# Kernel optimization log

Measured on AMD Instinct MI355X. Metric: run time of the kernel, lower is better.

Reference implementation:

```python
import jax, jax.numpy as jnp
import numpy as np
import math

B, N, DS, DP, DH, H, PQK, PV = 1, 384, 384, 128, 16, 12, 4, 8
PKV = PQK + PV
EPS = 1e-8
SOFTPLUS_INV_1 = 0.541324854612918


def setup_inputs() -> dict:
    key = jax.random.key(0)
    ks = jax.random.split(key, 20)
    W = lambda k, shp: (jax.random.normal(k, shp, dtype=jnp.float32) * 0.02)
    s = jax.random.normal(ks[0], (B, N, DS), dtype=jnp.float32)
    z = jax.random.normal(ks[1], (B, N, N, DP), dtype=jnp.float32)
    # random rigid frames: orthonormal rotations via QR + translations
    rot = jnp.linalg.qr(jax.random.normal(ks[2], (B, N, 3, 3), dtype=jnp.float32))[0]
    trans = jax.random.normal(ks[3], (B, N, 3), dtype=jnp.float32)
    square_mask = jnp.zeros((B, 1, N, N), dtype=jnp.float32)
    HC = H * DH
    COUT = H * (DP + DH + PV * 4)  # 2112
    return {
        "s": s, "z": z, "rot": rot, "trans": trans, "square_mask": square_mask,
        "Wq": W(ks[4], (DS, HC)), "bq": jnp.zeros((HC,), jnp.float32),
        "Wkv": W(ks[5], (DS, 2 * HC)), "bkv": jnp.zeros((2 * HC,), jnp.float32),
        "Wq_pts": W(ks[6], (DS, H * PQK * 3)), "bq_pts": jnp.zeros((H * PQK * 3,), jnp.float32),
        "Wkv_pts": W(ks[7], (DS, H * PKV * 3)), "bkv_pts": jnp.zeros((H * PKV * 3,), jnp.float32),
        "Wb": W(ks[8], (DP, H)), "bb": jnp.zeros((H,), jnp.float32),
        "head_weights": jnp.full((H,), SOFTPLUS_INV_1, dtype=jnp.float32),
        "Wout": W(ks[9], (COUT, DS)), "bout": jnp.zeros((DS,), jnp.float32),
    }


def _points(lin, rot, trans, npts):
    # lin: [B,N,3*H*npts] laid out as 3 coord-chunks of H*npts each (torch split+stack)
    pts = jnp.swapaxes(lin.reshape(B, N, 3, H * npts), -1, -2)  # [B,N,H*npts,3]
    pts = jnp.einsum('bnij,bnpj->bnpi', rot, pts) + trans[:, :, None, :]  # frame apply
    return pts.reshape(B, N, H, npts, 3)


def reference(s, z, rot, trans, square_mask, Wq, bq, Wkv, bkv, Wq_pts, bq_pts,
              Wkv_pts, bkv_pts, Wb, bb, head_weights, Wout, bout):
    q = (s @ Wq + bq).reshape(B, N, H, DH)
    kv = (s @ Wkv + bkv).reshape(B, N, H, 2 * DH)
    k, v = kv[..., :DH], kv[..., DH:]

    q_pts = _points(s @ Wq_pts + bq_pts, rot, trans, PQK)          # [B,N,H,PQK,3]
    kv_pts = _points(s @ Wkv_pts + bkv_pts, rot, trans, PKV)       # [B,N,H,PKV,3]
    k_pts, v_pts = kv_pts[..., :PQK, :], kv_pts[..., PQK:, :]

    bias = z @ Wb + bb                                             # [B,Nq,Nk,H]
    attn = jnp.einsum('bqhd,bkhd->bhqk', q, k) * math.sqrt(1.0 / (3 * DH))
    attn = attn + math.sqrt(1.0 / 3) * jnp.transpose(bias, (0, 3, 1, 2))

    diff = q_pts[:, :, None] - k_pts[:, None]                      # [B,Nq,Nk,H,PQK,3]
    dist2 = jnp.sum(diff * diff, axis=-1)                          # [B,Nq,Nk,H,PQK]
    hw = jax.nn.softplus(head_weights) * math.sqrt(1.0 / (3 * (PQK * 9.0 / 2)))
    pt_att = -0.5 * jnp.sum(dist2 * hw[None, None, None, :, None], axis=-1)  # [B,Nq,Nk,H]

    attn = attn + square_mask + jnp.transpose(pt_att, (0, 3, 1, 2))
    attn = jax.nn.softmax(attn, axis=-1)                           # [B,H,Nq,Nk]

    o = jnp.einsum('bhqk,bkhd->bqhd', attn, v).reshape(B, N, H * DH)
    o_pts = jnp.einsum('bhqk,bkhpc->bqhpc', attn, v_pts)           # [B,N,H,PV,3]
    # frame invert_apply: R^T (p - t)
    o_pts = jnp.einsum('bnji,bnhpj->bnhpi', rot, o_pts - trans[:, :, None, None, :])
    o_pts_norm = jnp.sqrt(jnp.sum(o_pts ** 2, axis=-1) + EPS).reshape(B, N, H * PV)
    o_pts_flat = o_pts.reshape(B, N, H * PV, 3)
    o_pair = jnp.einsum('bhqk,bqkc->bqhc', attn, z).reshape(B, N, H * DP)

    cat = jnp.concatenate(
        [o, o_pts_flat[..., 0], o_pts_flat[..., 1], o_pts_flat[..., 2], o_pts_norm, o_pair],
        axis=-1)
    return cat @ Wout + bout
```

## Files before the change

kernel.cpp:

```cpp
#include <hip/hip_runtime.h>
#include <math.h>

#define N     384
#define DSd   384
#define DP    128
#define DH    16
#define H     12
#define PQK   4
#define PV    8
#define HC    (H*DH)
#define PROJW 1152
#define NN    (N*N)
#define COUTD 2112
#define KSPL  4
#define KCH   96

__global__ __launch_bounds__(256) void pack_w(
    const float* __restrict__ Wq, const float* __restrict__ Wkv,
    const float* __restrict__ Wqp, const float* __restrict__ Wkvp,
    const float* __restrict__ bq, const float* __restrict__ bkv,
    const float* __restrict__ bqp, const float* __restrict__ bkvp,
    float* __restrict__ Wcat, float* __restrict__ bcat)
{
    const int i = blockIdx.x * 256 + threadIdx.x;
    if (i < DSd * PROJW) {
        const int r = i / PROJW, c = i % PROJW;
        float v;
        if (c < 192)      v = Wq[r*192 + c];
        else if (c < 576) v = Wkv[r*384 + (c-192)];
        else if (c < 720) v = Wqp[r*144 + (c-576)];
        else              v = Wkvp[r*432 + (c-720)];
        Wcat[i] = v;
    }
    if (i < PROJW) {
        float v;
        if (i < 192)      v = bq[i];
        else if (i < 576) v = bkv[i-192];
        else if (i < 720) v = bqp[i-576];
        else              v = bkvp[i-720];
        bcat[i] = v;
    }
}

__global__ __launch_bounds__(256) void gemm32x64(
    const float* __restrict__ A, const float* __restrict__ B,
    float* __restrict__ partial, int M, int Nc, int K, int kchunk)
{
    __shared__ float Ast[32][34];
    __shared__ float Bs[32][68];
    const int tid = threadIdx.x;
    const int tc = tid & 15, tr = tid >> 4;
    const int row0 = blockIdx.x * 32, col0 = blockIdx.y * 64;
    const int kbeg = blockIdx.z * kchunk;
    const int kend = kbeg + kchunk;
    float acc[2][4] = {};

    for (int kk = kbeg; kk < kend; kk += 32) {
        #pragma unroll
        for (int i = tid; i < 32*32; i += 256) {
            int r = i >> 5, c = i & 31;
            Ast[c][r] = A[(row0 + r) * K + kk + c];
        }
        #pragma unroll
        for (int i = tid; i < 32*64; i += 256) {
            int r = i >> 6, c = i & 63;
            Bs[r][c] = B[(kk + r) * Nc + col0 + c];
        }
        __syncthreads();
        #pragma unroll
        for (int p = 0; p < 32; ++p) {
            const float2 av = *(const float2*)&Ast[p][tr*2];
            const float4 bv = *(const float4*)&Bs[p][tc*4];
            acc[0][0] = fmaf(av.x, bv.x, acc[0][0]);
            acc[0][1] = fmaf(av.x, bv.y, acc[0][1]);
            acc[0][2] = fmaf(av.x, bv.z, acc[0][2]);
            acc[0][3] = fmaf(av.x, bv.w, acc[0][3]);
            acc[1][0] = fmaf(av.y, bv.x, acc[1][0]);
            acc[1][1] = fmaf(av.y, bv.y, acc[1][1]);
            acc[1][2] = fmaf(av.y, bv.z, acc[1][2]);
            acc[1][3] = fmaf(av.y, bv.w, acc[1][3]);
        }
        __syncthreads();
    }
    float* p0 = partial + ((size_t)blockIdx.z * M + row0 + tr*2) * Nc + col0 + tc*4;
    *(float4*)p0        = make_float4(acc[0][0], acc[0][1], acc[0][2], acc[0][3]);
    *(float4*)(p0 + Nc) = make_float4(acc[1][0], acc[1][1], acc[1][2], acc[1][3]);
}

__global__ __launch_bounds__(256) void reduce_kernel(
    const float* __restrict__ partial, const float* __restrict__ bias,
    float* __restrict__ out, int nc, int parts, int stride)
{
    const int i = blockIdx.x * 256 + threadIdx.x;
    float a = bias[i % nc];
    for (int t = 0; t < parts; ++t) a += partial[(size_t)t * stride + i];
    out[i] = a;
}

__global__ __launch_bounds__(192) void repack_kernel(
    const float* __restrict__ proj, const float* __restrict__ rot,
    const float* __restrict__ trans,
    float* __restrict__ q_t, float* __restrict__ k_t, float* __restrict__ vcat,
    float* __restrict__ qpts_t, float* __restrict__ kpts_t)
{
    const int n = blockIdx.x;
    const int tid = threadIdx.x;
    const float* pr = proj + n * PROJW;

    {
        int h = tid >> 4, d = tid & 15;
        q_t[(h*N + n)*DH + d]   = pr[h*DH + d];
        k_t[(h*N + n)*DH + d]   = pr[HC + h*2*DH + d];
        vcat[(h*N + n)*40 + d]  = pr[HC + h*2*DH + DH + d];
    }
    const float r00 = rot[n*9+0], r01 = rot[n*9+1], r02 = rot[n*9+2];
    const float r10 = rot[n*9+3], r11 = rot[n*9+4], r12 = rot[n*9+5];
    const float r20 = rot[n*9+6], r21 = rot[n*9+7], r22 = rot[n*9+8];
    const float t0 = trans[n*3+0], t1 = trans[n*3+1], t2 = trans[n*3+2];

    if (tid < H*PQK) {
        int p = tid;
        float l0 = pr[576 + 0*48 + p];
        float l1 = pr[576 + 1*48 + p];
        float l2 = pr[576 + 2*48 + p];
        int h = p / PQK, pt = p % PQK;
        float* dst = qpts_t + (h*N + n)*12 + pt*3;
        dst[0] = r00*l0 + r01*l1 + r02*l2 + t0;
        dst[1] = r10*l0 + r11*l1 + r12*l2 + t1;
        dst[2] = r20*l0 + r21*l1 + r22*l2 + t2;
    }
    if (tid < H*(PQK+PV)) {
        int p = tid;
        float l0 = pr[720 + 0*144 + p];
        float l1 = pr[720 + 1*144 + p];
        float l2 = pr[720 + 2*144 + p];
        int h = p / 12, pt = p % 12;
        float x0 = r00*l0 + r01*l1 + r02*l2 + t0;
        float x1 = r10*l0 + r11*l1 + r12*l2 + t1;
        float x2 = r20*l0 + r21*l1 + r22*l2 + t2;
        if (pt < PQK) {
            float* dst = kpts_t + (h*N + n)*12 + pt*3;
            dst[0] = x0; dst[1] = x1; dst[2] = x2;
        } else {
            float* dst = vcat + (h*N + n)*40 + 16 + (pt - PQK)*3;
            dst[0] = x0; dst[1] = x1; dst[2] = x2;
        }
    }
}

__global__ __launch_bounds__(256) void bias_kernel(
    const float* __restrict__ z, const float* __restrict__ Wb,
    const float* __restrict__ bb, float* __restrict__ biasattn)
{
    __shared__ float zt[64][DP+1];
    const int tid = threadIdx.x;
    const int base = blockIdx.x * 64;
    for (int i = tid; i < 64*DP; i += 256)
        zt[i >> 7][i & 127] = z[(size_t)base*DP + i];
    __syncthreads();

    const int p = tid & 63;
    const int g3 = __builtin_amdgcn_readfirstlane((tid >> 6) * 3);
    float a0 = 0.f, a1 = 0.f, a2 = 0.f;
    #pragma unroll 4
    for (int c = 0; c < DP; ++c) {
        float zv = zt[p][c];
        a0 = fmaf(zv, Wb[c*H + g3 + 0], a0);
        a1 = fmaf(zv, Wb[c*H + g3 + 1], a1);
        a2 = fmaf(zv, Wb[c*H + g3 + 2], a2);
    }
    const float sc = 0.5773502691896258f;
    const int pair = base + p;
    biasattn[(g3+0)*NN + pair] = (a0 + bb[g3+0]) * sc;
    biasattn[(g3+1)*NN + pair] = (a1 + bb[g3+1]) * sc;
    biasattn[(g3+2)*NN + pair] = (a2 + bb[g3+2]) * sc;
}

__global__ __launch_bounds__(128) void attn_kernel(
    const float* __restrict__ q_t, const float* __restrict__ k_t,
    const float* __restrict__ qpts_t, const float* __restrict__ kpts_t,
    const float* __restrict__ mask, const float* __restrict__ head_weights,
    float* __restrict__ biasattn)
{
    const int h  = blockIdx.x % H;
    const int qi = blockIdx.x / H;
    const int tid = threadIdx.x;
    __shared__ float logits[N];
    __shared__ float red[4];

    const float4* qv = (const float4*)(q_t + (h*N + qi)*DH);
    const float4 q0 = qv[0], q1 = qv[1], q2 = qv[2], q3 = qv[3];
    const float4* qpv = (const float4*)(qpts_t + (h*N + qi)*12);
    const float4 p0 = qpv[0], p1 = qpv[1], p2 = qpv[2];
    const float hw = log1pf(expf(head_weights[h])) * 0.13608276348795434f;

    float lmax = -1e30f;
    for (int k = tid; k < N; k += 128) {
        const float4* kr = (const float4*)(k_t + (h*N + k)*DH);
        const float4 a0 = kr[0], a1 = kr[1], a2 = kr[2], a3 = kr[3];
        float dot = q0.x*a0.x;
        dot = fmaf(q0.y, a0.y, dot); dot = fmaf(q0.z, a0.z, dot); dot = fmaf(q0.w, a0.w, dot);
        dot = fmaf(q1.x, a1.x, dot); dot = fmaf(q1.y, a1.y, dot); dot = fmaf(q1.z, a1.z, dot); dot = fmaf(q1.w, a1.w, dot);
        dot = fmaf(q2.x, a2.x, dot); dot = fmaf(q2.y, a2.y, dot); dot = fmaf(q2.z, a2.z, dot); dot = fmaf(q2.w, a2.w, dot);
        dot = fmaf(q3.x, a3.x, dot); dot = fmaf(q3.y, a3.y, dot); dot = fmaf(q3.z, a3.z, dot); dot = fmaf(q3.w, a3.w, dot);
        const float4* kp = (const float4*)(kpts_t + (h*N + k)*12);
        const float4 b0 = kp[0], b1 = kp[1], b2 = kp[2];
        float df, d2;
        df = p0.x-b0.x; d2 = df*df;
        df = p0.y-b0.y; d2 = fmaf(df, df, d2);
        df = p0.z-b0.z; d2 = fmaf(df, df, d2);
        df = p0.w-b0.w; d2 = fmaf(df, df, d2);
        df = p1.x-b1.x; d2 = fmaf(df, df, d2);
        df = p1.y-b1.y; d2 = fmaf(df, df, d2);
        df = p1.z-b1.z; d2 = fmaf(df, df, d2);
        df = p1.w-b1.w; d2 = fmaf(df, df, d2);
        df = p2.x-b2.x; d2 = fmaf(df, df, d2);
        df = p2.y-b2.y; d2 = fmaf(df, df, d2);
        df = p2.z-b2.z; d2 = fmaf(df, df, d2);
        df = p2.w-b2.w; d2 = fmaf(df, df, d2);
        float l = fmaf(dot, 0.14433756729740643f,
                       biasattn[h*NN + qi*N + k] + mask[qi*N + k])
                - 0.5f * hw * d2;
        logits[k] = l;
        lmax = fmaxf(lmax, l);
    }
    #pragma unroll
    for (int o = 32; o > 0; o >>= 1) lmax = fmaxf(lmax, __shfl_xor(lmax, o));
    if ((tid & 63) == 0) red[tid >> 6] = lmax;
    __syncthreads();
    const float m = fmaxf(red[0], red[1]);
    float lsum = 0.f;
    for (int k = tid; k < N; k += 128) {
        float e = __expf(logits[k] - m);
        logits[k] = e;
        lsum += e;
    }
    #pragma unroll
    for (int o = 32; o > 0; o >>= 1) lsum += __shfl_xor(lsum, o);
    if ((tid & 63) == 0) red[2 + (tid >> 6)] = lsum;
    __syncthreads();
    const float inv = 1.f / (red[2] + red[3]);
    for (int k = tid; k < N; k += 128)
        biasattn[h*NN + qi*N + k] = logits[k] * inv;
}

__global__ __launch_bounds__(256) void opair_partial(
    const float* __restrict__ attn, const float* __restrict__ vcat,
    const float* __restrict__ z, float* __restrict__ P1, float* __restrict__ P2)
{
    const int qi = blockIdx.x, kq = blockIdx.y;
    const int k0 = kq * KCH;
    const int tid = threadIdx.x;
    __shared__ float pzs[2][H][DP];

    {
        const int c = tid & 127;
        const int halfu = __builtin_amdgcn_readfirstlane(tid >> 7);
        const float* zp = z + ((size_t)qi*N + k0 + halfu*48)*DP + c;
        float zreg[48];
        #pragma unroll
        for (int k = 0; k < 48; ++k) zreg[k] = zp[(size_t)k*DP];
        const float* arow = attn + qi*N + k0 + halfu*48;
        #pragma unroll
        for (int h = 0; h < H; ++h) {
            float a = 0.f;
            #pragma unroll
            for (int k = 0; k < 48; ++k)
                a = fmaf(arow[h*NN + k], zreg[k], a);
            pzs[halfu][h][c] = a;
        }
    }
    {
        const int wv = tid >> 6, lane = tid & 63;
        if (lane < 40) {
            #pragma unroll
            for (int ih = 0; ih < 3; ++ih) {
                const int h = wv*3 + ih;
                const float* arow2 = attn + h*NN + qi*N + k0;
                const float* vp = vcat + ((size_t)h*N + k0)*40 + lane;
                float a = 0.f;
                #pragma unroll 4
                for (int k = 0; k < KCH; ++k)
                    a = fmaf(arow2[k], vp[k*40], a);
                const int j = (lane < 16) ? h*16 + lane : 192 + h*24 + (lane-16);
                P1[((size_t)qi*KSPL + kq)*480 + j] = a;
            }
        }
    }
    __syncthreads();
    for (int i = tid; i < H*DP; i += 256)
        P2[((size_t)qi*KSPL + kq)*(H*DP) + i] = pzs[0][i>>7][i&127] + pzs[1][i>>7][i&127];
}

__global__ __launch_bounds__(256) void combine_kernel(
    const float* __restrict__ P1, const float* __restrict__ P2,
    const float* __restrict__ rot, const float* __restrict__ trans,
    float* __restrict__ cat)
{
    const int qi = blockIdx.x;
    const int tid = threadIdx.x;
    __shared__ float catv[COUTD];
    __shared__ float praw[H*PV*3];

    for (int j = tid; j < 480; j += 256) {
        const float* p = P1 + (size_t)qi*KSPL*480 + j;
        float s = p[0] + p[480] + p[960] + p[1440];
        if (j < 192) catv[j] = s; else praw[j-192] = s;
    }
    for (int i = tid; i < H*DP; i += 256) {
        const float* p = P2 + (size_t)qi*KSPL*(H*DP) + i;
        catv[576 + i] = p[0] + p[1536] + p[3072] + p[4608];
    }
    __syncthreads();
    if (tid < H*PV) {
        const float* rr = rot + qi*9;
        const float t0 = trans[qi*3+0], t1 = trans[qi*3+1], t2 = trans[qi*3+2];
        float y0 = praw[tid*3+0] - t0;
        float y1 = praw[tid*3+1] - t1;
        float y2 = praw[tid*3+2] - t2;
        float f0 = rr[0]*y0 + rr[3]*y1 + rr[6]*y2;
        float f1 = rr[1]*y0 + rr[4]*y1 + rr[7]*y2;
        float f2 = rr[2]*y0 + rr[5]*y1 + rr[8]*y2;
        catv[HC + 0*96 + tid] = f0;
        catv[HC + 1*96 + tid] = f1;
        catv[HC + 2*96 + tid] = f2;
        catv[HC + 3*96 + tid] = sqrtf(f0*f0 + f1*f1 + f2*f2 + 1e-8f);
    }
    __syncthreads();
    float4* dst = (float4*)(cat + (size_t)qi * COUTD);
    const float4* src = (const float4*)catv;
    for (int i = tid; i < COUTD/4; i += 256) dst[i] = src[i];
}

extern "C" void kernel_launch(void* const* d_in, const int* in_sizes, int n_in,
                              void* d_out, int out_size, void* d_ws, size_t ws_size,
                              hipStream_t stream)
{
    const float* s       = (const float*)d_in[0];
    const float* z       = (const float*)d_in[1];
    const float* rot     = (const float*)d_in[2];
    const float* trans   = (const float*)d_in[3];
    const float* mask    = (const float*)d_in[4];
    const float* Wq      = (const float*)d_in[5];
    const float* bq      = (const float*)d_in[6];
    const float* Wkv     = (const float*)d_in[7];
    const float* bkv     = (const float*)d_in[8];
    const float* Wq_pts  = (const float*)d_in[9];
    const float* bq_pts  = (const float*)d_in[10];
    const float* Wkv_pts = (const float*)d_in[11];
    const float* bkv_pts = (const float*)d_in[12];
    const float* Wb      = (const float*)d_in[13];
    const float* bb      = (const float*)d_in[14];
    const float* hwts    = (const float*)d_in[15];
    const float* Wout    = (const float*)d_in[16];
    const float* bout    = (const float*)d_in[17];
    float* out = (float*)d_out;
    float* ws  = (float*)d_ws;

    float* ba     = ws;
    float* cat    = ba     + 1769472;
    float* q_t    = cat    + 811008;
    float* k_t    = q_t    + 73728;
    float* qpts_t = k_t    + 73728;
    float* kpts_t = qpts_t + 55296;
    float* vcat   = kpts_t + 55296;
    float* X      = vcat   + 184320;
    float* proj     = X;
    float* partialP = X + 442368;
    float* Wcat     = X + 1327104;
    float* bcat     = X + 1769472;
    float* P1       = X;
    float* P2       = X + 737280;
    float* partialF = X;

    pack_w<<<1728, 256, 0, stream>>>(Wq, Wkv, Wq_pts, Wkv_pts, bq, bkv, bq_pts, bkv_pts, Wcat, bcat);
    gemm32x64<<<dim3(12,18,2), 256, 0, stream>>>(s, Wcat, partialP, N, PROJW, DSd, 192);
    reduce_kernel<<<1728, 256, 0, stream>>>(partialP, bcat, proj, PROJW, 2, 442368);
    repack_kernel<<<N, 192, 0, stream>>>(proj, rot, trans, q_t, k_t, vcat, qpts_t, kpts_t);
    bias_kernel<<<NN/64, 256, 0, stream>>>(z, Wb, bb, ba);
    attn_kernel<<<N*H, 128, 0, stream>>>(q_t, k_t, qpts_t, kpts_t, mask, hwts, ba);
    opair_partial<<<dim3(N, KSPL), 256, 0, stream>>>(ba, vcat, z, P1, P2);
    combine_kernel<<<N, 256, 0, stream>>>(P1, P2, rot, trans, cat);
    gemm32x64<<<dim3(12,6,11), 256, 0, stream>>>(cat, Wout, partialF, N, 384, COUTD, 192);
    reduce_kernel<<<576, 256, 0, stream>>>(partialF, bout, out, 384, 11, NN);
}
```

Before: 278.4 us.

## Transpose vcat layout, per-pair bias kernel, and loop reordering in opair

vcat is stored channel-major ([h][40][N]), so the attn·v loop in opair_partial reads contiguous k for each lane, and three heads now accumulate in one loop. bias_kernel drops its shared-memory staging. Each thread handles one pair and computes all 12 heads from float4 loads of z, which means strided per-thread global reads. The z·attn loop in opair_partial streams z rows into 12 accumulators instead of holding 48 values in registers, which cuts register pressure.

```diff
diff --git a/kernel.cpp b/kernel.cpp
--- a/kernel.cpp
+++ b/kernel.cpp
@@ -109,9 +109,9 @@
 
     {
         int h = tid >> 4, d = tid & 15;
-        q_t[(h*N + n)*DH + d]   = pr[h*DH + d];
-        k_t[(h*N + n)*DH + d]   = pr[HC + h*2*DH + d];
-        vcat[(h*N + n)*40 + d]  = pr[HC + h*2*DH + DH + d];
+        q_t[(h*N + n)*DH + d]     = pr[h*DH + d];
+        k_t[(h*N + n)*DH + d]     = pr[HC + h*2*DH + d];
+        vcat[(h*40 + d)*N + n]    = pr[HC + h*2*DH + DH + d];
     }
     const float r00 = rot[n*9+0], r01 = rot[n*9+1], r02 = rot[n*9+2];
     const float r10 = rot[n*9+3], r11 = rot[n*9+4], r12 = rot[n*9+5];
@@ -142,8 +142,10 @@
             float* dst = kpts_t + (h*N + n)*12 + pt*3;
             dst[0] = x0; dst[1] = x1; dst[2] = x2;
         } else {
-            float* dst = vcat + (h*N + n)*40 + 16 + (pt - PQK)*3;
-            dst[0] = x0; dst[1] = x1; dst[2] = x2;
+            const int j = 16 + (pt - PQK)*3;
+            vcat[(h*40 + j+0)*N + n] = x0;
+            vcat[(h*40 + j+1)*N + n] = x1;
+            vcat[(h*40 + j+2)*N + n] = x2;
         }
     }
 }
@@ -152,28 +154,24 @@
     const float* __restrict__ z, const float* __restrict__ Wb,
     const float* __restrict__ bb, float* __restrict__ biasattn)
 {
-    __shared__ float zt[64][DP+1];
-    const int tid = threadIdx.x;
-    const int base = blockIdx.x * 64;
-    for (int i = tid; i < 64*DP; i += 256)
-        zt[i >> 7][i & 127] = z[(size_t)base*DP + i];
-    __syncthreads();
-
-    const int p = tid & 63;
-    const int g3 = __builtin_amdgcn_readfirstlane((tid >> 6) * 3);
-    float a0 = 0.f, a1 = 0.f, a2 = 0.f;
+    const int pair = blockIdx.x * 256 + threadIdx.x;
+    const float4* zp = (const float4*)(z + (size_t)pair * DP);
+    float acc[12] = {};
     #pragma unroll 4
-    for (int c = 0; c < DP; ++c) {
-        float zv = zt[p][c];
-        a0 = fmaf(zv, Wb[c*H + g3 + 0], a0);
-        a1 = fmaf(zv, Wb[c*H + g3 + 1], a1);
-        a2 = fmaf(zv, Wb[c*H + g3 + 2], a2);
+    for (int c4 = 0; c4 < DP/4; ++c4) {
+        const float4 zv = zp[c4];
+        #pragma unroll
+        for (int h = 0; h < H; ++h) {
+            acc[h] = fmaf(zv.x, Wb[(c4*4+0)*H + h], acc[h]);
+            acc[h] = fmaf(zv.y, Wb[(c4*4+1)*H + h], acc[h]);
+            acc[h] = fmaf(zv.z, Wb[(c4*4+2)*H + h], acc[h]);
+            acc[h] = fmaf(zv.w, Wb[(c4*4+3)*H + h], acc[h]);
+        }
     }
     const float sc = 0.5773502691896258f;
-    const int pair = base + p;
-    biasattn[(g3+0)*NN + pair] = (a0 + bb[g3+0]) * sc;
-    biasattn[(g3+1)*NN + pair] = (a1 + bb[g3+1]) * sc;
-    biasattn[(g3+2)*NN + pair] = (a2 + bb[g3+2]) * sc;
+    #pragma unroll
+    for (int h = 0; h < H; ++h)
+        biasattn[h*NN + pair] = (acc[h] + bb[h]) * sc;
 }
 
 __global__ __launch_bounds__(128) void attn_kernel(
@@ -255,36 +253,43 @@
 
     {
         const int c = tid & 127;
-        const int halfu = __builtin_amdgcn_readfirstlane(tid >> 7);
-        const float* zp = z + ((size_t)qi*N + k0 + halfu*48)*DP + c;
-        float zreg[48];
-        #pragma unroll
-        for (int k = 0; k < 48; ++k) zreg[k] = zp[(size_t)k*DP];
-        const float* arow = attn + qi*N + k0 + halfu*48;
-        #pragma unroll
-        for (int h = 0; h < H; ++h) {
-            float a = 0.f;
+        const int half = __builtin_amdgcn_readfirstlane(tid >> 7);
+        const float* zp = z + ((size_t)qi*N + k0 + half*48)*DP + c;
+        const float* arow = attn + qi*N + k0 + half*48;
+        float acc[12] = {};
+        #pragma unroll 4
+        for (int k = 0; k < 48; ++k) {
+            const float zv = zp[(size_t)k*DP];
             #pragma unroll
-            for (int k = 0; k < 48; ++k)
-                a = fmaf(arow[h*NN + k], zreg[k], a);
-            pzs[halfu][h][c] = a;
-        }
+            for (int h = 0; h < H; ++h)
+                acc[h] = fmaf(arow[h*NN + k], zv, acc[h]);
+        }
+        #pragma unroll
+        for (int h = 0; h < H; ++h) pzs[half][h][c] = acc[h];
     }
     {
-        const int wv = tid >> 6, lane = tid & 63;
+        const int wv = __builtin_amdgcn_readfirstlane(tid >> 6);
+        const int lane = tid & 63;
         if (lane < 40) {
-            #pragma unroll
-            for (int ih = 0; ih < 3; ++ih) {
-                const int h = wv*3 + ih;
-                const float* arow2 = attn + h*NN + qi*N + k0;
-                const float* vp = vcat + ((size_t)h*N + k0)*40 + lane;
-                float a = 0.f;
-                #pragma unroll 4
-                for (int k = 0; k < KCH; ++k)
-                    a = fmaf(arow2[k], vp[k*40], a);
-                const int j = (lane < 16) ? h*16 + lane : 192 + h*24 + (lane-16);
-                P1[((size_t)qi*KSPL + kq)*480 + j] = a;
+            const int h0 = wv*3;
+            const float* a0 = attn + (h0+0)*NN + qi*N + k0;
+            const float* a1 = attn + (h0+1)*NN + qi*N + k0;
+            const float* a2 = attn + (h0+2)*NN + qi*N + k0;
+            const float* v0 = vcat + ((h0+0)*40 + lane)*N + k0;
+            const float* v1 = vcat + ((h0+1)*40 + lane)*N + k0;
+            const float* v2 = vcat + ((h0+2)*40 + lane)*N + k0;
+            float s0 = 0.f, s1 = 0.f, s2 = 0.f;
+            #pragma unroll 4
+            for (int k = 0; k < KCH; ++k) {
+                s0 = fmaf(a0[k], v0[k], s0);
+                s1 = fmaf(a1[k], v1[k], s1);
+                s2 = fmaf(a2[k], v2[k], s2);
             }
+            float* pb = P1 + ((size_t)qi*KSPL + kq)*480;
+            const int j0 = (lane < 16) ? (h0+0)*16 + lane : 192 + (h0+0)*24 + (lane-16);
+            const int j1 = (lane < 16) ? (h0+1)*16 + lane : 192 + (h0+1)*24 + (lane-16);
+            const int j2 = (lane < 16) ? (h0+2)*16 + lane : 192 + (h0+2)*24 + (lane-16);
+            pb[j0] = s0; pb[j1] = s1; pb[j2] = s2;
         }
     }
     __syncthreads();
@@ -377,7 +382,7 @@
     gemm32x64<<<dim3(12,18,2), 256, 0, stream>>>(s, Wcat, partialP, N, PROJW, DSd, 192);
     reduce_kernel<<<1728, 256, 0, stream>>>(partialP, bcat, proj, PROJW, 2, 442368);
     repack_kernel<<<N, 192, 0, stream>>>(proj, rot, trans, q_t, k_t, vcat, qpts_t, kpts_t);
-    bias_kernel<<<NN/64, 256, 0, stream>>>(z, Wb, bb, ba);
+    bias_kernel<<<NN/256, 256, 0, stream>>>(z, Wb, bb, ba);
     attn_kernel<<<N*H, 128, 0, stream>>>(q_t, k_t, qpts_t, kpts_t, mask, hwts, ba);
     opair_partial<<<dim3(N, KSPL), 256, 0, stream>>>(ba, vcat, z, P1, P2);
     combine_kernel<<<N, 256, 0, stream>>>(P1, P2, rot, trans, cat);
```

After: 319.4 us. 14.7% more time.
